# Performance work log

Hardware: AMD Instinct MI355X
Metric: run time of the kernel (lower is better)

The kernel has to match this reference:

```python
import jax, jax.numpy as jnp
import numpy as np

B, HG, WG, D, NH, K = 4, 32, 32, 768, 12, 7
HD = D // NH  # 64


def _neigh_idx(H, W, k):
    # NATTEN semantics: 7x7 window centered at the query, shifted (clamped)
    # at borders so every query has exactly k*k neighbors.
    si = np.clip(np.arange(H) - k // 2, 0, H - k)  # [H] window row starts
    sj = np.clip(np.arange(W) - k // 2, 0, W - k)  # [W] window col starts
    ri = si[:, None] + np.arange(k)[None, :]       # [H, k]
    cj = sj[:, None] + np.arange(k)[None, :]       # [W, k]
    idx = ri[:, None, :, None] * W + cj[None, :, None, :]  # [H, W, k, k]
    return jnp.asarray(idx.reshape(H * W, k * k), dtype=jnp.int32)


def setup_inputs() -> dict:
    key = jax.random.key(0)
    ks = jax.random.split(key, 3)
    s = D ** -0.5
    return {
        "x": jax.random.normal(ks[0], (B, HG * WG, D), dtype=jnp.float32),
        "qkv_w": jax.random.normal(ks[1], (3 * D, D), dtype=jnp.float32) * s,
        "qkv_b": jnp.zeros((3 * D,), dtype=jnp.float32),
        "proj_w": jax.random.normal(ks[2], (D, D), dtype=jnp.float32) * s,
        "proj_b": jnp.zeros((D,), dtype=jnp.float32),
    }


def reference(x, qkv_w, qkv_b, proj_w, proj_b):
    b, n, d = x.shape  # n == HG*WG
    idx = _neigh_idx(HG, WG, K)  # [n, K*K] flat neighbor token indices

    qkv = x @ qkv_w.T + qkv_b                      # [b, n, 3d]
    q, k, v = jnp.split(qkv, 3, axis=-1)
    q = q.reshape(b, n, NH, HD) * (HD ** -0.5)     # [b, n, h, hd]
    k = k.reshape(b, n, NH, HD)
    v = v.reshape(b, n, NH, HD)

    kn = jnp.take(k, idx, axis=1)                  # [b, n, 49, h, hd]
    vn = jnp.take(v, idx, axis=1)                  # [b, n, 49, h, hd]

    scores = jnp.einsum('bnhd,bnkhd->bnhk', q, kn)  # [b, n, h, 49]
    attn = jax.nn.softmax(scores, axis=-1)
    out = jnp.einsum('bnhk,bnkhd->bnhd', attn, vn).reshape(b, n, d)
    return out @ proj_w.T + proj_b
```

## Files before the change

### kernel.cpp

```cpp
#include <hip/hip_runtime.h>


typedef __bf16 bf16x8 __attribute__((ext_vector_type(8)));
typedef short s16x4 __attribute__((ext_vector_type(4)));
typedef float f32x4 __attribute__((ext_vector_type(4)));

__device__ __forceinline__ unsigned short f2bf(float f) {
  unsigned u = __float_as_uint(f);
  u += 0x7fffu + ((u >> 16) & 1u);
  return (unsigned short)(u >> 16);
}

template <typename T>
__device__ __forceinline__ void gld_lds16(const T* g, T* l) {
  __builtin_amdgcn_global_load_lds((const __attribute__((address_space(1))) void*)g,
                                   (__attribute__((address_space(3))) void*)l, 16, 0, 0);
}

__global__ void cvt_kernel(const float* __restrict__ x, const float* __restrict__ w1,
                           const float* __restrict__ w2, unsigned short* __restrict__ xo,
                           unsigned short* __restrict__ w1o, unsigned short* __restrict__ w2o) {
  const int n1 = 4096 * 768 / 4;
  const int n2 = 2304 * 768 / 4;
  const int n3 = 768 * 768 / 4;
  int i = blockIdx.x * 256 + threadIdx.x;
  float4 v;
  unsigned short* dst;
  int o;
  if (i < n1) {
    o = i; v = ((const float4*)x)[o]; dst = xo;
  } else if (i < n1 + n2) {
    o = i - n1; v = ((const float4*)w1)[o]; dst = w1o;
  } else if (i < n1 + n2 + n3) {
    o = i - n1 - n2; v = ((const float4*)w2)[o]; dst = w2o;
  } else {
    return;
  }
  ushort4 r;
  r.x = f2bf(v.x); r.y = f2bf(v.y); r.z = f2bf(v.z); r.w = f2bf(v.w);
  ((ushort4*)dst)[o] = r;
}

template <int MODE>
__global__ __launch_bounds__(256) void gemm_bt(const unsigned short* __restrict__ A,
                                               const unsigned short* __restrict__ Bm,
                                               const float* __restrict__ bias,
                                               unsigned short* __restrict__ obf,
                                               unsigned short* __restrict__ vtout,
                                               float* __restrict__ of32,
                                               int M, int N, int Kd) {
  __shared__ __align__(16) unsigned short sA[128 * 32];
  __shared__ __align__(16) unsigned short sB[128 * 32];
  const int tid = threadIdx.x;
  const int lane = tid & 63;
  const int wv = tid >> 6;
  const int m0 = blockIdx.y * 128, n0 = blockIdx.x * 128;
  const int wrow = (wv >> 1) * 64, wcol = (wv & 1) * 64;
  const int lr = lane & 15, lq = lane >> 4;

  f32x4 acc[4][4] = {};

  const unsigned short* gA = A + (size_t)(m0 + (tid >> 2)) * Kd + (tid & 3) * 8;
  const unsigned short* gB = Bm + (size_t)(n0 + (tid >> 2)) * Kd + (tid & 3) * 8;

  for (int k0 = 0; k0 < Kd; k0 += 32) {
    gld_lds16(gA + k0, sA + tid * 8);
    gld_lds16(gA + (size_t)64 * Kd + k0, sA + 2048 + tid * 8);
    gld_lds16(gB + k0, sB + tid * 8);
    gld_lds16(gB + (size_t)64 * Kd + k0, sB + 2048 + tid * 8);
    __syncthreads();

    bf16x8 af[4], bfr[4];
#pragma unroll
    for (int t = 0; t < 4; ++t) {
      af[t] = *(const bf16x8*)(sA + (wrow + t * 16 + lr) * 32 + lq * 8);
      bfr[t] = *(const bf16x8*)(sB + (wcol + t * 16 + lr) * 32 + lq * 8);
    }
#pragma unroll
    for (int im = 0; im < 4; ++im)
#pragma unroll
      for (int in = 0; in < 4; ++in)
        acc[im][in] = __builtin_amdgcn_mfma_f32_16x16x32_bf16(af[im], bfr[in], acc[im][in], 0, 0, 0);
    __syncthreads();
  }

  if (MODE == 0) {
    const int sidx = n0 / 768;
    if (sidx == 2) {
#pragma unroll
      for (int im = 0; im < 4; ++im) {
#pragma unroll
        for (int in = 0; in < 4; ++in) {
          int gn = n0 + wcol + in * 16 + lr;
          int rem = gn - 1536;
          int hh = rem >> 6, dd = gn & 63;
          float bsv = bias[gn];
          int gm0 = m0 + wrow + im * 16 + lq * 4;
          ushort4 pk;
          pk.x = f2bf(acc[im][in][0] + bsv);
          pk.y = f2bf(acc[im][in][1] + bsv);
          pk.z = f2bf(acc[im][in][2] + bsv);
          pk.w = f2bf(acc[im][in][3] + bsv);
          *(ushort4*)(vtout + (size_t)(hh * 64 + dd) * 4096 + gm0) = pk;
        }
      }
    } else {
      const float scale = (sidx == 0) ? 0.18033688f : 1.0f;
#pragma unroll
      for (int im = 0; im < 4; ++im) {
#pragma unroll
        for (int in = 0; in < 4; ++in) {
          int gn = n0 + wcol + in * 16 + lr;
          int rem = gn - sidx * 768;
          int hh = rem >> 6, dd = gn & 63;
          float bsv = bias[gn];
#pragma unroll
          for (int r = 0; r < 4; ++r) {
            int gm = m0 + wrow + im * 16 + lq * 4 + r;
            float val = (acc[im][in][r] + bsv) * scale;
            obf[((size_t)(sidx * 12 + hh) * 4096 + gm) * 64 + dd] = f2bf(val);
          }
        }
      }
    }
  } else {
#pragma unroll
    for (int im = 0; im < 4; ++im) {
#pragma unroll
      for (int in = 0; in < 4; ++in) {
        int gn = n0 + wcol + in * 16 + lr;
        float bsv = bias[gn];
#pragma unroll
        for (int r = 0; r < 4; ++r) {
          int gm = m0 + wrow + im * 16 + lq * 4 + r;
          of32[(size_t)gm * N + gn] = acc[im][in][r] + bsv;
        }
      }
    }
  }
}

__global__ __launch_bounds__(256, 2) void natten_kernel(const unsigned short* __restrict__ qkvt,
                                                        unsigned short* __restrict__ aout) {
  __shared__ __align__(16) unsigned short sQ[64 * 64];
  __shared__ __align__(16) unsigned short sK[256 * 64];
  __shared__ __align__(16) unsigned short sVt[64 * 256];
  const int h = blockIdx.x, ip = blockIdx.y, b = blockIdx.z;
  const int i0 = ip * 2;
  const int tid = threadIdx.x, lane = tid & 63, wv = tid >> 6;
  const int lg = lane >> 4, lm = lane & 15;
  int si0 = i0 - 3; si0 = si0 < 0 ? 0 : si0; if (si0 > 25) si0 = 25;
  const int gb = b * 1024;
  const unsigned short* Qg = qkvt + ((size_t)h * 4096 + gb + i0 * 32) * 64;
  const unsigned short* Kg = qkvt + ((size_t)(12 + h) * 4096 + gb) * 64;
  const unsigned short* Vg = qkvt + (size_t)24 * 4096 * 64 + (size_t)h * 64 * 4096 + gb;

#pragma unroll
  for (int it = 0; it < 2; ++it) {
    int f = it * 256 + tid;
    int q = f >> 3, c16 = f & 7;
    uint4 v = *(const uint4*)(Qg + q * 64 + c16 * 8);
    int s = q & 15;
    *(uint2*)(sQ + q * 64 + ((((c16 << 1)) ^ s) << 2)) = make_uint2(v.x, v.y);
    *(uint2*)(sQ + q * 64 + ((((c16 << 1) | 1) ^ s) << 2)) = make_uint2(v.z, v.w);
  }
#pragma unroll
  for (int it = 0; it < 8; ++it) {
    int f = it * 256 + tid;
    int t = f >> 3, c16 = f & 7;
    int wr = t >> 5, c = t & 31;
    int row = si0 + wr; if (row > 31) row = 31;
    uint4 v = *(const uint4*)(Kg + (row * 32 + c) * 64 + c16 * 8);
    int s = t & 15;
    *(uint2*)(sK + t * 64 + ((((c16 << 1)) ^ s) << 2)) = make_uint2(v.x, v.y);
    *(uint2*)(sK + t * 64 + ((((c16 << 1) | 1) ^ s) << 2)) = make_uint2(v.z, v.w);
  }
#pragma unroll
  for (int it = 0; it < 8; ++it) {
    int f = it * 256 + tid;
    int d = f >> 5, tc16 = f & 31;
    int wr = tc16 >> 2;
    int row = si0 + wr; if (row > 31) row = 31;
    uint4 v = *(const uint4*)(Vg + (size_t)d * 4096 + row * 32 + (tc16 & 3) * 8);
    int s = d & 15;
    *(uint2*)(sVt + d * 256 + ((((tc16 << 1)) ^ s) << 2)) = make_uint2(v.x, v.y);
    *(uint2*)(sVt + d * 256 + ((((tc16 << 1) | 1) ^ s) << 2)) = make_uint2(v.z, v.w);
  }
  __syncthreads();

  const int row_sel = wv >> 1;
  const int jhalf = wv & 1;
  const int i = i0 + row_sel;
  int si_w = i - 3; si_w = si_w < 0 ? 0 : si_w; if (si_w > 25) si_w = 25;
  const int toff = (si_w - si0) * 32;
  const int j = jhalf * 16 + lm;
  int sj = j - 3; sj = sj < 0 ? 0 : sj; if (sj > 25) sj = 25;

  float madd[2][4];
#pragma unroll
  for (int p = 0; p < 2; ++p)
#pragma unroll
    for (int r = 0; r < 4; ++r) {
      int c = p * 16 + lg * 4 + r;
      madd[p][r] = (c >= sj && c <= sj + 6) ? 0.f : -1e30f;
    }

  s16x4 qf[4];
  const int qrow = row_sel * 32 + j;
#pragma unroll
  for (int ks = 0; ks < 4; ++ks)
    qf[ks] = *(const s16x4*)(sQ + qrow * 64 + ((((ks << 2) + lg) ^ (qrow & 15)) << 2));

  f32x4 accS[14];
#pragma unroll
  for (int tt = 0; tt < 14; ++tt) {
    f32x4 a = {0.f, 0.f, 0.f, 0.f};
    const int trow = toff + tt * 16 + lm;
    const unsigned short* kr = sK + trow * 64;
    const int sw = trow & 15;
#pragma unroll
    for (int ks = 0; ks < 4; ++ks) {
      s16x4 kf = *(const s16x4*)(kr + ((((ks << 2) + lg) ^ sw) << 2));
      a = __builtin_amdgcn_mfma_f32_16x16x16bf16_1k(kf, qf[ks], a, 0, 0, 0);
    }
    accS[tt] = a;
  }

  float mx = -3e38f;
#pragma unroll
  for (int tt = 0; tt < 14; ++tt)
#pragma unroll
    for (int r = 0; r < 4; ++r) {
      float v = accS[tt][r] + madd[tt & 1][r];
      accS[tt][r] = v;
      mx = fmaxf(mx, v);
    }
  mx = fmaxf(mx, __shfl_xor(mx, 16, 64));
  mx = fmaxf(mx, __shfl_xor(mx, 32, 64));
  float sum = 0.f;
#pragma unroll
  for (int tt = 0; tt < 14; ++tt)
#pragma unroll
    for (int r = 0; r < 4; ++r) {
      float p = exp2f(accS[tt][r] - mx);
      accS[tt][r] = p;
      sum += p;
    }
  sum += __shfl_xor(sum, 16, 64);
  sum += __shfl_xor(sum, 32, 64);
  const float inv = 1.f / sum;

  s16x4 pf[14];
#pragma unroll
  for (int tt = 0; tt < 14; ++tt) {
    union { unsigned u[2]; s16x4 v; } pk;
    pk.u[0] = ((unsigned)f2bf(accS[tt][1]) << 16) | f2bf(accS[tt][0]);
    pk.u[1] = ((unsigned)f2bf(accS[tt][3]) << 16) | f2bf(accS[tt][2]);
    pf[tt] = pk.v;
  }

  f32x4 accO[4] = {};
  const int choff = toff >> 2;
#pragma unroll
  for (int tt = 0; tt < 14; ++tt) {
    const int c8 = choff + tt * 4 + lg;
#pragma unroll
    for (int nt = 0; nt < 4; ++nt) {
      const int d = nt * 16 + lm;
      s16x4 vf = *(const s16x4*)(sVt + d * 256 + ((c8 ^ (d & 15)) << 2));
      accO[nt] = __builtin_amdgcn_mfma_f32_16x16x16bf16_1k(pf[tt], vf, accO[nt], 0, 0, 0);
    }
  }

  float invr[4];
#pragma unroll
  for (int r = 0; r < 4; ++r) invr[r] = __shfl(inv, lg * 4 + r, 64);

  const int tokbase = gb + i * 32 + jhalf * 16;
#pragma unroll
  for (int nt = 0; nt < 4; ++nt)
#pragma unroll
    for (int r = 0; r < 4; ++r) {
      int tok = tokbase + lg * 4 + r;
      aout[(size_t)tok * 768 + h * 64 + nt * 16 + lm] = f2bf(accO[nt][r] * invr[r]);
    }
}

extern "C" void kernel_launch(void* const* d_in, const int* in_sizes, int n_in,
                              void* d_out, int out_size, void* d_ws, size_t ws_size,
                              hipStream_t stream) {
  const float* x      = (const float*)d_in[0];
  const float* qkv_w  = (const float*)d_in[1];
  const float* qkv_b  = (const float*)d_in[2];
  const float* proj_w = (const float*)d_in[3];
  const float* proj_b = (const float*)d_in[4];
  char* ws = (char*)d_ws;

  unsigned short* xb    = (unsigned short*)(ws);
  unsigned short* wqkv  = (unsigned short*)(ws + 6291456);
  unsigned short* wproj = (unsigned short*)(ws + 9830400);
  unsigned short* qkvt  = (unsigned short*)(ws + 11010048);
  unsigned short* attnb = (unsigned short*)(ws + 29884416);
  unsigned short* vt    = qkvt + (size_t)24 * 4096 * 64;
  float* out = (float*)d_out;

  cvt_kernel<<<5376, 256, 0, stream>>>(x, qkv_w, proj_w, xb, wqkv, wproj);
  gemm_bt<0><<<dim3(18, 32), 256, 0, stream>>>(xb, wqkv, qkv_b, qkvt, vt, nullptr, 4096, 2304, 768);
  natten_kernel<<<dim3(12, 16, 4), 256, 0, stream>>>(qkvt, attnb);
  gemm_bt<1><<<dim3(6, 32), 256, 0, stream>>>(attnb, wproj, proj_b, nullptr, nullptr, out, 4096, 768, 768);
}
```

Baseline: 155.6 us.

## Double-buffer GEMM LDS tiles, swizzle LDS chunks, and remap blocks across XCDs

The GEMM now keeps two LDS buffers and issues the next K-slice's global-to-LDS loads before the MFMA work on the current slice, so load latency can overlap compute. LDS chunk positions are XOR-swizzled on both the store and the fragment read to reduce bank conflicts. Block indices are also remapped so each XCD works on a contiguous group of tiles for better L2 locality. The extra LDS doubles shared memory per block, which may reduce occupancy. The remap hardcodes grid shapes per mode (9x8 or 3x8 tile groups per XCD pair), which ties it to these problem sizes.

After: 145.2 us. 1.07x faster.

```diff
diff --git a/kernel.cpp b/kernel.cpp
--- a/kernel.cpp
+++ b/kernel.cpp
@@ -49,32 +49,54 @@
                                                unsigned short* __restrict__ vtout,
                                                float* __restrict__ of32,
                                                int M, int N, int Kd) {
-  __shared__ __align__(16) unsigned short sA[128 * 32];
-  __shared__ __align__(16) unsigned short sB[128 * 32];
+  __shared__ __align__(16) unsigned short sA[2][128 * 32];
+  __shared__ __align__(16) unsigned short sB[2][128 * 32];
   const int tid = threadIdx.x;
   const int lane = tid & 63;
   const int wv = tid >> 6;
-  const int m0 = blockIdx.y * 128, n0 = blockIdx.x * 128;
+
+  constexpr int HX = (MODE == 0) ? 9 : 3;
+  constexpr int HY = 8;
+  const int lin = blockIdx.y * gridDim.x + blockIdx.x;
+  const int xcd = lin & 7, rrr = lin >> 3;
+  const int bx = (xcd & 1) * HX + rrr % HX;
+  const int by = (xcd >> 1) * HY + rrr / HX;
+  const int m0 = by * 128, n0 = bx * 128;
+
   const int wrow = (wv >> 1) * 64, wcol = (wv & 1) * 64;
   const int lr = lane & 15, lq = lane >> 4;
+  const int rchunk = (lq ^ ((lr >> 1) & 3)) * 8;
 
   f32x4 acc[4][4] = {};
 
-  const unsigned short* gA = A + (size_t)(m0 + (tid >> 2)) * Kd + (tid & 3) * 8;
-  const unsigned short* gB = Bm + (size_t)(n0 + (tid >> 2)) * Kd + (tid & 3) * 8;
-
+  const int schunk = ((tid & 3) ^ ((tid >> 3) & 3)) * 8;
+  const unsigned short* gA = A + (size_t)(m0 + (tid >> 2)) * Kd + schunk;
+  const unsigned short* gB = Bm + (size_t)(n0 + (tid >> 2)) * Kd + schunk;
+
+  gld_lds16(gA, &sA[0][tid * 8]);
+  gld_lds16(gA + (size_t)64 * Kd, &sA[0][2048 + tid * 8]);
+  gld_lds16(gB, &sB[0][tid * 8]);
+  gld_lds16(gB + (size_t)64 * Kd, &sB[0][2048 + tid * 8]);
+  __syncthreads();
+
+  int cur = 0;
   for (int k0 = 0; k0 < Kd; k0 += 32) {
-    gld_lds16(gA + k0, sA + tid * 8);
-    gld_lds16(gA + (size_t)64 * Kd + k0, sA + 2048 + tid * 8);
-    gld_lds16(gB + k0, sB + tid * 8);
-    gld_lds16(gB + (size_t)64 * Kd + k0, sB + 2048 + tid * 8);
-    __syncthreads();
-
+    const int nxt = k0 + 32;
+    if (nxt < Kd) {
+      unsigned short* dA = sA[cur ^ 1];
+      unsigned short* dB = sB[cur ^ 1];
+      gld_lds16(gA + nxt, dA + tid * 8);
+      gld_lds16(gA + (size_t)64 * Kd + nxt, dA + 2048 + tid * 8);
+      gld_lds16(gB + nxt, dB + tid * 8);
+      gld_lds16(gB + (size_t)64 * Kd + nxt, dB + 2048 + tid * 8);
+    }
+    const unsigned short* cA = sA[cur];
+    const unsigned short* cB = sB[cur];
     bf16x8 af[4], bfr[4];
 #pragma unroll
     for (int t = 0; t < 4; ++t) {
-      af[t] = *(const bf16x8*)(sA + (wrow + t * 16 + lr) * 32 + lq * 8);
-      bfr[t] = *(const bf16x8*)(sB + (wcol + t * 16 + lr) * 32 + lq * 8);
+      af[t] = *(const bf16x8*)(cA + (wrow + t * 16 + lr) * 32 + rchunk);
+      bfr[t] = *(const bf16x8*)(cB + (wcol + t * 16 + lr) * 32 + rchunk);
     }
 #pragma unroll
     for (int im = 0; im < 4; ++im)
@@ -82,6 +104,7 @@
       for (int in = 0; in < 4; ++in)
         acc[im][in] = __builtin_amdgcn_mfma_f32_16x16x32_bf16(af[im], bfr[in], acc[im][in], 0, 0, 0);
     __syncthreads();
+    cur ^= 1;
   }
 
   if (MODE == 0) {
```

## Triple-buffer GEMM LDS tiles, swizzle LDS, remap blocks per XCD, shrink proj tiles

Applied to the files above, without the earlier changes.

The GEMM kernel now uses a three-stage LDS ring with async global-to-LDS loads issued two tiles ahead. Explicit vmcnt waits and a single barrier per step replace the two syncthreads, so loads overlap the MFMA work. An XOR swizzle on the 16-byte chunk index is meant to cut LDS bank conflicts. Block indices are remapped so blocks that land on the same XCD share nearby tiles, and the projection GEMM switches to 64x64 tiles to launch more blocks. The trade-offs are more LDS per block, which can lower occupancy, and hand-written waitcnt logic that relies on the exact number of outstanding loads.

Measured after the change: 135.8 us. 12.7% less time.

```diff
diff --git a/kernel.cpp b/kernel.cpp
--- a/kernel.cpp
+++ b/kernel.cpp
@@ -41,7 +41,7 @@
   ((ushort4*)dst)[o] = r;
 }
 
-template <int MODE>
+template <int MODE, int BM, int BN>
 __global__ __launch_bounds__(256) void gemm_bt(const unsigned short* __restrict__ A,
                                                const unsigned short* __restrict__ Bm,
                                                const float* __restrict__ bias,
@@ -49,48 +49,90 @@
                                                unsigned short* __restrict__ vtout,
                                                float* __restrict__ of32,
                                                int M, int N, int Kd) {
-  __shared__ __align__(16) unsigned short sA[128 * 32];
-  __shared__ __align__(16) unsigned short sB[128 * 32];
+  constexpr int RA = BM / 64, RB = BN / 64;
+  constexpr int MI = BM / 32, NI = BN / 32;
+  constexpr int L = RA + RB;
+  __shared__ __align__(16) unsigned short sA[3][BM * 32];
+  __shared__ __align__(16) unsigned short sB[3][BN * 32];
   const int tid = threadIdx.x;
   const int lane = tid & 63;
   const int wv = tid >> 6;
-  const int m0 = blockIdx.y * 128, n0 = blockIdx.x * 128;
-  const int wrow = (wv >> 1) * 64, wcol = (wv & 1) * 64;
+
+  constexpr int HX = (MODE == 0) ? 9 : 6;
+  constexpr int HY = (MODE == 0) ? 8 : 16;
+  const int lin = blockIdx.y * gridDim.x + blockIdx.x;
+  const int xcd = lin & 7, rrr = lin >> 3;
+  const int bx = (xcd & 1) * HX + rrr % HX;
+  const int by = (xcd >> 1) * HY + rrr / HX;
+  const int m0 = by * BM, n0 = bx * BN;
+
+  const int wrow = (wv >> 1) * (BM / 2), wcol = (wv & 1) * (BN / 2);
   const int lr = lane & 15, lq = lane >> 4;
-
-  f32x4 acc[4][4] = {};
-
-  const unsigned short* gA = A + (size_t)(m0 + (tid >> 2)) * Kd + (tid & 3) * 8;
-  const unsigned short* gB = Bm + (size_t)(n0 + (tid >> 2)) * Kd + (tid & 3) * 8;
-
-  for (int k0 = 0; k0 < Kd; k0 += 32) {
-    gld_lds16(gA + k0, sA + tid * 8);
-    gld_lds16(gA + (size_t)64 * Kd + k0, sA + 2048 + tid * 8);
-    gld_lds16(gB + k0, sB + tid * 8);
-    gld_lds16(gB + (size_t)64 * Kd + k0, sB + 2048 + tid * 8);
-    __syncthreads();
-
-    bf16x8 af[4], bfr[4];
-#pragma unroll
-    for (int t = 0; t < 4; ++t) {
-      af[t] = *(const bf16x8*)(sA + (wrow + t * 16 + lr) * 32 + lq * 8);
-      bfr[t] = *(const bf16x8*)(sB + (wcol + t * 16 + lr) * 32 + lq * 8);
-    }
-#pragma unroll
-    for (int im = 0; im < 4; ++im)
-#pragma unroll
-      for (int in = 0; in < 4; ++in)
+  const int rchunk = (lq ^ ((lr >> 1) & 3)) * 8;
+
+  f32x4 acc[MI][NI] = {};
+
+  const int schunk = ((tid & 3) ^ ((tid >> 3) & 3)) * 8;
+  const unsigned short* gA = A + (size_t)(m0 + (tid >> 2)) * Kd + schunk;
+  const unsigned short* gB = Bm + (size_t)(n0 + (tid >> 2)) * Kd + schunk;
+
+  const int NS = Kd >> 5;
+
+#define STAGE_TILE(tile, bufidx)                                                          \
+  do {                                                                                    \
+    const int _off = (tile) * 32;                                                         \
+    unsigned short* _dA = sA[(bufidx)];                                                   \
+    unsigned short* _dB = sB[(bufidx)];                                                   \
+    _Pragma("unroll")                                                                     \
+    for (int _r = 0; _r < RA; ++_r)                                                       \
+      gld_lds16(gA + (size_t)(_r * 64) * Kd + _off, _dA + _r * 2048 + tid * 8);           \
+    _Pragma("unroll")                                                                     \
+    for (int _r = 0; _r < RB; ++_r)                                                       \
+      gld_lds16(gB + (size_t)(_r * 64) * Kd + _off, _dB + _r * 2048 + tid * 8);           \
+  } while (0)
+
+  STAGE_TILE(0, 0);
+  STAGE_TILE(1, 1);
+  __builtin_amdgcn_sched_barrier(0);
+  if constexpr (L == 4) asm volatile("s_waitcnt vmcnt(4) lgkmcnt(0)" ::: "memory");
+  else                  asm volatile("s_waitcnt vmcnt(2) lgkmcnt(0)" ::: "memory");
+  __builtin_amdgcn_s_barrier();
+
+  for (int step = 0; step < NS; ++step) {
+    const unsigned short* cA = sA[step % 3];
+    const unsigned short* cB = sB[step % 3];
+    bf16x8 af[MI], bfr[NI];
+#pragma unroll
+    for (int t = 0; t < MI; ++t) af[t] = *(const bf16x8*)(cA + (wrow + t * 16 + lr) * 32 + rchunk);
+#pragma unroll
+    for (int t = 0; t < NI; ++t) bfr[t] = *(const bf16x8*)(cB + (wcol + t * 16 + lr) * 32 + rchunk);
+
+    if (step + 2 < NS) STAGE_TILE(step + 2, (step + 2) % 3);
+
+#pragma unroll
+    for (int im = 0; im < MI; ++im)
+#pragma unroll
+      for (int in = 0; in < NI; ++in)
         acc[im][in] = __builtin_amdgcn_mfma_f32_16x16x32_bf16(af[im], bfr[in], acc[im][in], 0, 0, 0);
-    __syncthreads();
-  }
+
+    __builtin_amdgcn_sched_barrier(0);
+    if (step < NS - 2) {
+      if constexpr (L == 4) asm volatile("s_waitcnt vmcnt(4) lgkmcnt(0)" ::: "memory");
+      else                  asm volatile("s_waitcnt vmcnt(2) lgkmcnt(0)" ::: "memory");
+    } else {
+      asm volatile("s_waitcnt vmcnt(0) lgkmcnt(0)" ::: "memory");
+    }
+    __builtin_amdgcn_s_barrier();
+  }
+#undef STAGE_TILE
 
   if (MODE == 0) {
     const int sidx = n0 / 768;
     if (sidx == 2) {
 #pragma unroll
-      for (int im = 0; im < 4; ++im) {
-#pragma unroll
-        for (int in = 0; in < 4; ++in) {
+      for (int im = 0; im < MI; ++im) {
+#pragma unroll
+        for (int in = 0; in < NI; ++in) {
           int gn = n0 + wcol + in * 16 + lr;
           int rem = gn - 1536;
           int hh = rem >> 6, dd = gn & 63;
@@ -107,9 +149,9 @@
     } else {
       const float scale = (sidx == 0) ? 0.18033688f : 1.0f;
 #pragma unroll
-      for (int im = 0; im < 4; ++im) {
-#pragma unroll
-        for (int in = 0; in < 4; ++in) {
+      for (int im = 0; im < MI; ++im) {
+#pragma unroll
+        for (int in = 0; in < NI; ++in) {
           int gn = n0 + wcol + in * 16 + lr;
           int rem = gn - sidx * 768;
           int hh = rem >> 6, dd = gn & 63;
@@ -125,9 +167,9 @@
     }
   } else {
 #pragma unroll
-    for (int im = 0; im < 4; ++im) {
-#pragma unroll
-      for (int in = 0; in < 4; ++in) {
+    for (int im = 0; im < MI; ++im) {
+#pragma unroll
+      for (int in = 0; in < NI; ++in) {
         int gn = n0 + wcol + in * 16 + lr;
         float bsv = bias[gn];
 #pragma unroll
@@ -305,7 +347,7 @@
   float* out = (float*)d_out;
 
   cvt_kernel<<<5376, 256, 0, stream>>>(x, qkv_w, proj_w, xb, wqkv, wproj);
-  gemm_bt<0><<<dim3(18, 32), 256, 0, stream>>>(xb, wqkv, qkv_b, qkvt, vt, nullptr, 4096, 2304, 768);
+  gemm_bt<0, 128, 128><<<dim3(18, 32), 256, 0, stream>>>(xb, wqkv, qkv_b, qkvt, vt, nullptr, 4096, 2304, 768);
   natten_kernel<<<dim3(12, 16, 4), 256, 0, stream>>>(qkvt, attnb);
-  gemm_bt<1><<<dim3(6, 32), 256, 0, stream>>>(attnb, wproj, proj_b, nullptr, nullptr, out, 4096, 768, 768);
-}
+  gemm_bt<1, 64, 64><<<dim3(12, 64), 256, 0, stream>>>(attnb, wproj, proj_b, nullptr, nullptr, out, 4096, 768, 768);
+}
```
